# Kernel tuning notes

Measured on AMD Instinct MI355X. Metric: run time of the kernel, lower is better.

The kernel has to match this reference:

```python
import jax, jax.numpy as jnp
import numpy as np

D = 1024
EPS = 1e-5  # torch LayerNorm default


def setup_inputs() -> dict:
    key = jax.random.key(0)
    ks = jax.random.split(key, 10)
    B, S = 4, 2048
    s = 1.0 / np.sqrt(D)
    inp = {
        "x": jax.random.normal(ks[0], (B, S, D), dtype=jnp.float32),
        "gamma": jnp.ones((D,), jnp.float32),
        "beta": jnp.zeros((D,), jnp.float32),
        "Wq": jax.random.normal(ks[1], (D, D), jnp.float32) * s,
        "bq": jax.random.normal(ks[2], (D,), jnp.float32) * 0.01,
        "Wk": jax.random.normal(ks[3], (D, D), jnp.float32) * s,
        "bk": jax.random.normal(ks[4], (D,), jnp.float32) * 0.01,
        "Wv": jax.random.normal(ks[5], (D, D), jnp.float32) * s,
        "bv": jax.random.normal(ks[6], (D,), jnp.float32) * 0.01,
        "Wo": jax.random.normal(ks[7], (D, D), jnp.float32) * s,
        "bo": jax.random.normal(ks[8], (D,), jnp.float32) * 0.01,
    }
    return inp


def reference(x, gamma, beta, Wq, bq, Wk, bk, Wv, bv, Wo, bo):
    # Pre-LayerNorm
    mu = jnp.mean(x, axis=-1, keepdims=True)
    var = jnp.mean(jnp.square(x - mu), axis=-1, keepdims=True)
    xn = (x - mu) * jax.lax.rsqrt(var + EPS) * gamma + beta
    # QKV projections (torch Linear: y = x @ W.T + b)
    Q = jnp.einsum('bsd,ed->bse', xn, Wq) + bq
    K = jnp.einsum('bsd,ed->bse', xn, Wk) + bk
    V = jnp.einsum('bsd,ed->bse', xn, Wv) + bv
    # Single-head full attention, scaled by sqrt(D); dropout inactive (eval)
    scores = jnp.einsum('bqd,bkd->bqk', Q, K) / jnp.sqrt(jnp.float32(D))
    attn = jax.nn.softmax(scores, axis=-1)
    out = jnp.einsum('bqk,bkd->bqd', attn, V)
    return jnp.einsum('bsd,ed->bse', out, Wo) + bo
```

## Files before the change

kernel.cpp:

```cpp
#include <hip/hip_runtime.h>
#include <hip/hip_bf16.h>
#include <stdint.h>

typedef __attribute__((ext_vector_type(4))) float f32x4;
typedef __attribute__((ext_vector_type(8))) __bf16 bf16x8;
typedef __attribute__((ext_vector_type(8))) unsigned short ushort8;

#define DEV static __device__ __forceinline__

__device__ __align__(4096) unsigned char g_scratch[125829120];

DEV unsigned short f2bf(float f) {
  union { float f; uint32_t u; } x; x.f = f;
  uint32_t u = x.u;
  uint32_t r = (u + 0x7fffu + ((u >> 16) & 1u)) >> 16;
  return (unsigned short)r;
}
DEV float bf2f(unsigned short b) {
  union { uint32_t u; float f; } x; x.u = ((uint32_t)b) << 16;
  return x.f;
}

DEV void gload16(const void* g, void* l) {
  __builtin_amdgcn_global_load_lds((const __attribute__((address_space(1))) void*)g,
                                   (__attribute__((address_space(3))) void*)l,
                                   16, 0, 0);
}

DEV int swz(int b) { return b ^ (((b >> 7) & 7) << 4); }

template<int OP>
__global__ __launch_bounds__(256, 2)
void gemm_bt(const unsigned short* __restrict__ A, const unsigned short* __restrict__ B,
             void* __restrict__ C,
             const float* __restrict__ bs0, const float* __restrict__ bs1,
             const float* __restrict__ bs2,
             int ldA, int ldB, int ldC, int K,
             long sAz, long sBz, long sCz)
{
  __shared__ unsigned short lds[16384];
  const int tid  = threadIdx.x;
  const int lane = tid & 63;
  const int wave = tid >> 6;
  const int z  = blockIdx.z;
  const int m0 = blockIdx.x * 128;
  const int n0 = blockIdx.y * 128;
  const unsigned short* Az = A + (size_t)z * sAz;
  const unsigned short* Bz = B + (size_t)z * sBz;
  const int wm = (wave >> 1) * 64;
  const int wn = (wave & 1) * 64;

  int aOff[4], bOff[4];
#pragma unroll
  for (int m = 0; m < 4; ++m) {
    int ar = wm + m * 16 + (lane & 15);
    aOff[m] = (ar * 128 + ((lane >> 4) * 16)) ^ ((ar & 7) << 4);
    int br = wn + m * 16 + (lane & 15);
    bOff[m] = ((br * 128 + ((lane >> 4) * 16)) ^ ((br & 7) << 4)) + 16384;
  }

  f32x4 acc[4][4] = {};

  const unsigned short* a_t = Az + (size_t)m0 * ldA;
  const unsigned short* b_t = Bz + (size_t)n0 * ldB;

  for (int kt = 0; kt < K; kt += 64) {
#pragma unroll
    for (int i = 0; i < 4; ++i) {
      int o = i * 4096 + tid * 16;
      int p = swz(o);
      int row = p >> 7;
      int ce  = (p & 127) >> 1;
      gload16(a_t + (size_t)row * ldA + (kt + ce), (char*)lds + o);
      gload16(b_t + (size_t)row * ldB + (kt + ce), (char*)lds + 16384 + o);
    }
    __syncthreads();
#pragma unroll
    for (int h = 0; h < 2; ++h) {
      bf16x8 av[4], bv4[4];
#pragma unroll
      for (int m = 0; m < 4; ++m)
        av[m] = *(const bf16x8*)((const char*)lds + (aOff[m] ^ (h << 6)));
#pragma unroll
      for (int n = 0; n < 4; ++n)
        bv4[n] = *(const bf16x8*)((const char*)lds + (bOff[n] ^ (h << 6)));
#pragma unroll
      for (int m = 0; m < 4; ++m)
#pragma unroll
        for (int n = 0; n < 4; ++n)
          acc[m][n] = __builtin_amdgcn_mfma_f32_16x16x32_bf16(av[m], bv4[n], acc[m][n], 0, 0, 0);
    }
    __syncthreads();
  }

  const int r0 = (lane >> 4) * 4;
  const int cL = lane & 15;

  if (OP == 0) {
    const float* bias = (z == 0) ? bs0 : ((z == 1) ? bs1 : bs2);
    if (z < 2) {
      const float scale = (z == 0) ? 0.03125f : 1.0f;
      unsigned short* Cp = (unsigned short*)C + (size_t)z * sCz;
#pragma unroll
      for (int n = 0; n < 4; ++n) {
        int colg = n0 + wn + n * 16 + cL;
        float bb = bias[colg];
#pragma unroll
        for (int m = 0; m < 4; ++m) {
          int rowg = m0 + wm + m * 16 + r0;
#pragma unroll
          for (int i = 0; i < 4; ++i)
            Cp[(size_t)(rowg + i) * ldC + colg] = f2bf((acc[m][n][i] + bb) * scale);
        }
      }
    } else {
      unsigned short* Vt = (unsigned short*)C + (size_t)2 * sCz;
#pragma unroll
      for (int n = 0; n < 4; ++n) {
        int colg = n0 + wn + n * 16 + cL;
        float bb = bias[colg];
#pragma unroll
        for (int m = 0; m < 4; ++m) {
          int rowg = m0 + wm + m * 16 + r0;
          int bat = rowg >> 11, s = rowg & 2047;
          ushort4 pk;
          pk.x = f2bf(acc[m][n][0] + bb);
          pk.y = f2bf(acc[m][n][1] + bb);
          pk.z = f2bf(acc[m][n][2] + bb);
          pk.w = f2bf(acc[m][n][3] + bb);
          *(ushort4*)(Vt + (size_t)bat * 2097152 + (size_t)colg * 2048 + s) = pk;
        }
      }
    }
  } else if (OP == 3) {
    float* Cp = (float*)C;
#pragma unroll
    for (int n = 0; n < 4; ++n) {
      int colg = n0 + wn + n * 16 + cL;
      float bb = bs0[colg];
#pragma unroll
      for (int m = 0; m < 4; ++m) {
        int rowg = m0 + wm + m * 16 + r0;
#pragma unroll
        for (int i = 0; i < 4; ++i)
          Cp[(size_t)(rowg + i) * ldC + colg] = acc[m][n][i] + bb;
      }
    }
  } else {
    unsigned short* Cp = (unsigned short*)C + (size_t)z * sCz;
#pragma unroll
    for (int n = 0; n < 4; ++n) {
      int colg = n0 + wn + n * 16 + cL;
#pragma unroll
      for (int m = 0; m < 4; ++m) {
        int rowg = m0 + wm + m * 16 + r0;
#pragma unroll
        for (int i = 0; i < 4; ++i)
          Cp[(size_t)(rowg + i) * ldC + colg] = f2bf(acc[m][n][i]);
      }
    }
  }
}

__global__ __launch_bounds__(256)
void cvt_w(const float* __restrict__ w0, const float* __restrict__ w1,
           const float* __restrict__ w2, const float* __restrict__ w3,
           unsigned short* __restrict__ dst)
{
  const float* src = (blockIdx.y == 0) ? w0 : (blockIdx.y == 1) ? w1
                   : (blockIdx.y == 2) ? w2 : w3;
  const int idx = (blockIdx.x * 256 + threadIdx.x) * 8;
  const float4 a = *(const float4*)(src + idx);
  const float4 b = *(const float4*)(src + idx + 4);
  unsigned short* d = dst + (size_t)blockIdx.y * 1048576 + idx;
  ushort4 r0, r1;
  r0.x = f2bf(a.x); r0.y = f2bf(a.y); r0.z = f2bf(a.z); r0.w = f2bf(a.w);
  r1.x = f2bf(b.x); r1.y = f2bf(b.y); r1.z = f2bf(b.z); r1.w = f2bf(b.w);
  *(ushort4*)(d) = r0;
  *(ushort4*)(d + 4) = r1;
}

__global__ __launch_bounds__(256)
void ln_kernel(const float* __restrict__ x, const float* __restrict__ gamma,
               const float* __restrict__ beta, unsigned short* __restrict__ xn)
{
  const int row = blockIdx.x;
  const int tid = threadIdx.x;
  const float4 xv = ((const float4*)(x + (size_t)row * 1024))[tid];
  float s = xv.x + xv.y + xv.z + xv.w;
#pragma unroll
  for (int d = 1; d < 64; d <<= 1) s += __shfl_xor(s, d);
  __shared__ float red1[4], red2[4];
  const int lane = tid & 63, wv = tid >> 6;
  if (lane == 0) red1[wv] = s;
  __syncthreads();
  const float mu = (red1[0] + red1[1] + red1[2] + red1[3]) * (1.0f / 1024.0f);
  float4 dv;
  dv.x = xv.x - mu; dv.y = xv.y - mu; dv.z = xv.z - mu; dv.w = xv.w - mu;
  float vs = dv.x * dv.x + dv.y * dv.y + dv.z * dv.z + dv.w * dv.w;
#pragma unroll
  for (int d = 1; d < 64; d <<= 1) vs += __shfl_xor(vs, d);
  if (lane == 0) red2[wv] = vs;
  __syncthreads();
  const float var = (red2[0] + red2[1] + red2[2] + red2[3]) * (1.0f / 1024.0f);
  const float rs = rsqrtf(var + 1e-5f);
  const float4 g = ((const float4*)gamma)[tid];
  const float4 b = ((const float4*)beta)[tid];
  ushort4 o;
  o.x = f2bf(dv.x * rs * g.x + b.x);
  o.y = f2bf(dv.y * rs * g.y + b.y);
  o.z = f2bf(dv.z * rs * g.z + b.z);
  o.w = f2bf(dv.w * rs * g.w + b.w);
  ((ushort4*)(xn + (size_t)row * 1024))[tid] = o;
}

__global__ __launch_bounds__(256)
void softmax_kernel(unsigned short* __restrict__ S)
{
  const size_t row = blockIdx.x;
  unsigned short* p = S + row * 2048;
  const int tid = threadIdx.x;
  ushort8 v = ((const ushort8*)p)[tid];
  float f[8];
#pragma unroll
  for (int j = 0; j < 8; ++j) f[j] = bf2f(v[j]);
  float mx = f[0];
#pragma unroll
  for (int j = 1; j < 8; ++j) mx = fmaxf(mx, f[j]);
#pragma unroll
  for (int d = 1; d < 64; d <<= 1) mx = fmaxf(mx, __shfl_xor(mx, d));
  __shared__ float rmax[4], rsum[4];
  const int lane = tid & 63, wv = tid >> 6;
  if (lane == 0) rmax[wv] = mx;
  __syncthreads();
  const float M = fmaxf(fmaxf(rmax[0], rmax[1]), fmaxf(rmax[2], rmax[3]));
  float e[8], sum = 0.f;
#pragma unroll
  for (int j = 0; j < 8; ++j) { e[j] = __expf(f[j] - M); sum += e[j]; }
#pragma unroll
  for (int d = 1; d < 64; d <<= 1) sum += __shfl_xor(sum, d);
  if (lane == 0) rsum[wv] = sum;
  __syncthreads();
  const float inv = 1.0f / (rsum[0] + rsum[1] + rsum[2] + rsum[3]);
#pragma unroll
  for (int j = 0; j < 8; ++j) v[j] = f2bf(e[j] * inv);
  ((ushort8*)p)[tid] = v;
}

extern "C" void kernel_launch(void* const* d_in, const int* in_sizes, int n_in,
                              void* d_out, int out_size, void* d_ws, size_t ws_size,
                              hipStream_t stream) {
  const float* x     = (const float*)d_in[0];
  const float* gamma = (const float*)d_in[1];
  const float* beta  = (const float*)d_in[2];
  const float* Wq    = (const float*)d_in[3];
  const float* bq    = (const float*)d_in[4];
  const float* Wk    = (const float*)d_in[5];
  const float* bk    = (const float*)d_in[6];
  const float* Wv    = (const float*)d_in[7];
  const float* bv    = (const float*)d_in[8];
  const float* Wo    = (const float*)d_in[9];
  const float* bo    = (const float*)d_in[10];

  char* ws;
  if (ws_size >= (size_t)125829120) {
    ws = (char*)d_ws;
  } else {
    void* sp = nullptr;
    hipGetSymbolAddress(&sp, HIP_SYMBOL(g_scratch));
    ws = (char*)sp;
  }

  unsigned short* xn  = (unsigned short*)(ws);
  unsigned short* qkv = (unsigned short*)(ws + 16777216);
  unsigned short* att = (unsigned short*)(ws + 67108864);
  unsigned short* wbf = (unsigned short*)(ws + 83886080);
  unsigned short* S   = (unsigned short*)(ws + 92274688);

  cvt_w<<<dim3(512, 4, 1), 256, 0, stream>>>(Wq, Wk, Wv, Wo, wbf);
  ln_kernel<<<8192, 256, 0, stream>>>(x, gamma, beta, xn);
  gemm_bt<0><<<dim3(64, 8, 3), 256, 0, stream>>>(
      xn, wbf, qkv, bq, bk, bv,
      1024, 1024, 1024, 1024, 0L, 1048576L, 8388608L);
  gemm_bt<1><<<dim3(16, 16, 4), 256, 0, stream>>>(
      qkv, qkv + 8388608, S, nullptr, nullptr, nullptr,
      1024, 1024, 2048, 1024, 2097152L, 2097152L, 4194304L);
  softmax_kernel<<<8192, 256, 0, stream>>>(S);
  gemm_bt<2><<<dim3(16, 8, 4), 256, 0, stream>>>(
      S, qkv + 16777216, att, nullptr, nullptr, nullptr,
      2048, 2048, 1024, 2048, 4194304L, 2097152L, 2097152L);
  gemm_bt<3><<<dim3(64, 8, 1), 256, 0, stream>>>(
      att, wbf + 3145728, d_out, bo, nullptr, nullptr,
      1024, 1024, 1024, 1024, 0L, 0L, 0L);
}
```

Before: 186.8 us.

## Add 256x256-tile 512-thread pipelined GEMM for QKV and score GEMMs

Adds a new GEMM kernel with 256x256 output tiles, 8 waves per block and 128 KB of dynamic LDS. It double-buffers K-chunks with interleaved global-to-LDS loads, manual waitcnt and barriers, and setprio around the MFMA blocks. The kernel replaces the 128-tile GEMM for the QKV projection and the QK^T scores, with a fallback if the large LDS attribute cannot be set. The larger tiles raise operand reuse and cut global traffic, at the cost of fewer blocks per launch (384 and 256) and a tighter hand-written barrier schedule.

```diff
diff --git a/kernel.cpp b/kernel.cpp
--- a/kernel.cpp
+++ b/kernel.cpp
@@ -162,6 +162,174 @@
   }
 }
 
+template<int OP>
+__global__ __launch_bounds__(512, 2)
+void gemm256(const unsigned short* __restrict__ A, const unsigned short* __restrict__ B,
+             void* __restrict__ C,
+             const float* __restrict__ bs0, const float* __restrict__ bs1,
+             const float* __restrict__ bs2,
+             int ldA, int ldB, int ldC, int K,
+             long sAz, long sBz, long sCz)
+{
+  extern __shared__ char lds[];
+  const int tid  = threadIdx.x;
+  const int lane = tid & 63;
+  const int wave = tid >> 6;
+  const int wr = wave >> 2;
+  const int wc = wave & 3;
+  const int z  = blockIdx.z;
+  const int m0 = blockIdx.x * 256;
+  const int n0 = blockIdx.y * 256;
+  const unsigned short* a_t = A + (size_t)z * sAz + (size_t)m0 * ldA;
+  const unsigned short* b_t = B + (size_t)z * sBz + (size_t)n0 * ldB;
+
+  const int so0 = tid * 16;        const int sp0 = swz(so0);
+  const int sr0 = sp0 >> 7, sc0 = (sp0 & 127) >> 1;
+  const int so1 = 8192 + tid * 16; const int sp1 = swz(so1);
+  const int sr1 = sp1 >> 7, sc1 = (sp1 & 127) >> 1;
+
+  int aoff[8];
+#pragma unroll
+  for (int mi = 0; mi < 8; ++mi) {
+    int r = mi * 16 + (lane & 15);
+    aoff[mi] = (r * 128 + ((lane >> 4) * 16)) ^ ((r & 7) << 4);
+  }
+  int boff[4];
+#pragma unroll
+  for (int ni = 0; ni < 4; ++ni) {
+    int r = (wc & 1) * 64 + ni * 16 + (lane & 15);
+    boff[ni] = (r * 128 + ((lane >> 4) * 16)) ^ ((r & 7) << 4);
+  }
+
+  f32x4 acc[8][4] = {};
+
+  auto STAGE = [&](int base, const unsigned short* src, int ld, int kc) {
+    gload16(src + sr0 * ld + kc + sc0, lds + base + so0);
+    gload16(src + sr1 * ld + kc + sc1, lds + base + so1);
+  };
+
+  const int NI = K >> 7;
+  STAGE(32768,  b_t,             ldB, 0);
+  STAGE(49152,  b_t + 128 * ldB, ldB, 0);
+  STAGE(0,      a_t,             ldA, 0);
+  STAGE(16384,  a_t + 128 * ldA, ldA, 0);
+  STAGE(98304,  b_t,             ldB, 64);
+  STAGE(114688, b_t + 128 * ldB, ldB, 64);
+
+  for (int it = 0; it < NI; ++it) {
+    const int kA1 = it * 128 + 64;
+    int kn  = it * 128 + 128; if (kn  > K - 64) kn  = K - 64;
+    int kn2 = it * 128 + 192; if (kn2 > K - 64) kn2 = K - 64;
+#pragma unroll
+    for (int c = 0; c < 2; ++c) {
+      const char* aB = lds + c * 65536 + wr * 16384;
+      const char* bB = lds + c * 65536 + 32768 + (wc >> 1) * 16384;
+      bf16x8 bfr[4][2];
+#pragma unroll
+      for (int s = 0; s < 4; ++s) {
+        const int p = c * 4 + s;
+        bf16x8 afr[2][2];
+        if (s == 0) {
+          if (p == 0) STAGE(65536, a_t, ldA, kA1);
+          else        STAGE(0,     a_t, ldA, kn);
+          asm volatile("s_waitcnt vmcnt(6)" ::: "memory");
+          asm volatile("s_barrier" ::: "memory");
+#pragma unroll
+          for (int ni = 0; ni < 4; ++ni)
+#pragma unroll
+            for (int h = 0; h < 2; ++h)
+              bfr[ni][h] = *(const bf16x8*)(bB + (boff[ni] ^ (h << 6)));
+#pragma unroll
+          for (int m2 = 0; m2 < 2; ++m2)
+#pragma unroll
+            for (int h = 0; h < 2; ++h)
+              afr[m2][h] = *(const bf16x8*)(aB + (aoff[m2] ^ (h << 6)));
+        } else {
+#pragma unroll
+          for (int m2 = 0; m2 < 2; ++m2)
+#pragma unroll
+            for (int h = 0; h < 2; ++h)
+              afr[m2][h] = *(const bf16x8*)(aB + (aoff[s * 2 + m2] ^ (h << 6)));
+          if (p == 1)      STAGE(81920,  a_t + 128 * ldA, ldA, kA1);
+          else if (p == 2) STAGE(32768,  b_t,             ldB, kn);
+          else if (p == 3) STAGE(49152,  b_t + 128 * ldB, ldB, kn);
+          else if (p == 5) STAGE(16384,  a_t + 128 * ldA, ldA, kn);
+          else if (p == 6) STAGE(98304,  b_t,             ldB, kn2);
+          else             STAGE(114688, b_t + 128 * ldB, ldB, kn2);
+          asm volatile("s_barrier" ::: "memory");
+        }
+        __builtin_amdgcn_s_setprio(1);
+#pragma unroll
+        for (int h = 0; h < 2; ++h)
+#pragma unroll
+          for (int ni = 0; ni < 4; ++ni)
+#pragma unroll
+            for (int m2 = 0; m2 < 2; ++m2)
+              acc[s * 2 + m2][ni] = __builtin_amdgcn_mfma_f32_16x16x32_bf16(
+                  afr[m2][h], bfr[ni][h], acc[s * 2 + m2][ni], 0, 0, 0);
+        __builtin_amdgcn_s_setprio(0);
+        asm volatile("s_barrier" ::: "memory");
+      }
+    }
+  }
+
+  const int r0 = (lane >> 4) * 4;
+  const int cL = lane & 15;
+  const int wrow = m0 + wr * 128;
+  const int wcol = n0 + wc * 64;
+
+  if (OP == 0) {
+    const float* bias = (z == 0) ? bs0 : ((z == 1) ? bs1 : bs2);
+    if (z < 2) {
+      const float scale = (z == 0) ? 0.03125f : 1.0f;
+      unsigned short* Cp = (unsigned short*)C + (size_t)z * sCz;
+#pragma unroll
+      for (int ni = 0; ni < 4; ++ni) {
+        int colg = wcol + ni * 16 + cL;
+        float bb = bias[colg];
+#pragma unroll
+        for (int mi = 0; mi < 8; ++mi) {
+          int rowg = wrow + mi * 16 + r0;
+#pragma unroll
+          for (int i = 0; i < 4; ++i)
+            Cp[(size_t)(rowg + i) * ldC + colg] = f2bf((acc[mi][ni][i] + bb) * scale);
+        }
+      }
+    } else {
+      unsigned short* Vt = (unsigned short*)C + (size_t)2 * sCz;
+#pragma unroll
+      for (int ni = 0; ni < 4; ++ni) {
+        int colg = wcol + ni * 16 + cL;
+        float bb = bias[colg];
+#pragma unroll
+        for (int mi = 0; mi < 8; ++mi) {
+          int rowg = wrow + mi * 16 + r0;
+          int bat = rowg >> 11, sdx = rowg & 2047;
+          ushort4 pk;
+          pk.x = f2bf(acc[mi][ni][0] + bb);
+          pk.y = f2bf(acc[mi][ni][1] + bb);
+          pk.z = f2bf(acc[mi][ni][2] + bb);
+          pk.w = f2bf(acc[mi][ni][3] + bb);
+          *(ushort4*)(Vt + (size_t)bat * 2097152 + (size_t)colg * 2048 + sdx) = pk;
+        }
+      }
+    }
+  } else {
+    unsigned short* Cp = (unsigned short*)C + (size_t)z * sCz;
+#pragma unroll
+    for (int ni = 0; ni < 4; ++ni) {
+      int colg = wcol + ni * 16 + cL;
+#pragma unroll
+      for (int mi = 0; mi < 8; ++mi) {
+        int rowg = wrow + mi * 16 + r0;
+#pragma unroll
+        for (int i = 0; i < 4; ++i)
+          Cp[(size_t)(rowg + i) * ldC + colg] = f2bf(acc[mi][ni][i]);
+      }
+    }
+  }
+}
+
 __global__ __launch_bounds__(256)
 void cvt_w(const float* __restrict__ w0, const float* __restrict__ w1,
            const float* __restrict__ w2, const float* __restrict__ w3,
@@ -277,15 +445,38 @@
   unsigned short* wbf = (unsigned short*)(ws + 83886080);
   unsigned short* S   = (unsigned short*)(ws + 92274688);
 
+  int use256 = 1;
+  if (hipFuncSetAttribute(reinterpret_cast<const void*>(&gemm256<0>),
+                          hipFuncAttributeMaxDynamicSharedMemorySize, 131072) != hipSuccess)
+    use256 = 0;
+  if (use256 &&
+      hipFuncSetAttribute(reinterpret_cast<const void*>(&gemm256<1>),
+                          hipFuncAttributeMaxDynamicSharedMemorySize, 131072) != hipSuccess)
+    use256 = 0;
+
   cvt_w<<<dim3(512, 4, 1), 256, 0, stream>>>(Wq, Wk, Wv, Wo, wbf);
   ln_kernel<<<8192, 256, 0, stream>>>(x, gamma, beta, xn);
-  gemm_bt<0><<<dim3(64, 8, 3), 256, 0, stream>>>(
-      xn, wbf, qkv, bq, bk, bv,
-      1024, 1024, 1024, 1024, 0L, 1048576L, 8388608L);
-  gemm_bt<1><<<dim3(16, 16, 4), 256, 0, stream>>>(
-      qkv, qkv + 8388608, S, nullptr, nullptr, nullptr,
-      1024, 1024, 2048, 1024, 2097152L, 2097152L, 4194304L);
+
+  if (use256)
+    gemm256<0><<<dim3(32, 4, 3), 512, 131072, stream>>>(
+        xn, wbf, qkv, bq, bk, bv,
+        1024, 1024, 1024, 1024, 0L, 1048576L, 8388608L);
+  else
+    gemm_bt<0><<<dim3(64, 8, 3), 256, 0, stream>>>(
+        xn, wbf, qkv, bq, bk, bv,
+        1024, 1024, 1024, 1024, 0L, 1048576L, 8388608L);
+
+  if (use256)
+    gemm256<1><<<dim3(8, 8, 4), 512, 131072, stream>>>(
+        qkv, qkv + 8388608, S, nullptr, nullptr, nullptr,
+        1024, 1024, 2048, 1024, 2097152L, 2097152L, 4194304L);
+  else
+    gemm_bt<1><<<dim3(16, 16, 4), 256, 0, stream>>>(
+        qkv, qkv + 8388608, S, nullptr, nullptr, nullptr,
+        1024, 1024, 2048, 1024, 2097152L, 2097152L, 4194304L);
+
   softmax_kernel<<<8192, 256, 0, stream>>>(S);
+
   gemm_bt<2><<<dim3(16, 8, 4), 256, 0, stream>>>(
       S, qkv + 16777216, att, nullptr, nullptr, nullptr,
       2048, 2048, 1024, 2048, 4194304L, 2097152L, 2097152L);
```

Result: slower. 214.5 us (+14.8%).
